# Optimization experiments

Hardware: AMD Instinct MI355X
Metric: run time of the kernel (lower is better)

## Reference

```python
import jax, jax.numpy as jnp
import numpy as np

N = 100000   # nodes
E = 1600000  # edges (before self loops)
IN, HID, OUT = 128, 128, 64


def setup_inputs() -> dict:
    key = jax.random.key(0)
    ks = jax.random.split(key, 5)
    x = jax.random.normal(ks[0], (N, IN), dtype=jnp.float32)
    edge_index = jax.random.randint(ks[1], (2, E), 0, N, dtype=jnp.int32)
    W1 = jax.random.normal(ks[2], (IN, HID), dtype=jnp.float32) * (1.0 / np.sqrt(IN))
    b1 = jnp.zeros((HID,), dtype=jnp.float32)
    W2 = jax.random.normal(ks[3], (HID, OUT), dtype=jnp.float32) * (1.0 / np.sqrt(HID))
    b2 = jnp.zeros((OUT,), dtype=jnp.float32)
    return {"x": x, "edge_index": edge_index, "W1": W1, "b1": b1, "W2": W2, "b2": b2}


def _gcn_conv(x, W, b, src, dst, norm):
    # linear transform first (small GEMM), then normalized scatter-add aggregation
    h = x @ W                                   # [N, d_out]
    msg = h[src] * norm[:, None]                # [E+N, d_out] gathered messages
    agg = jax.ops.segment_sum(msg, dst, num_segments=N)
    return agg + b


def reference(x, edge_index, W1, b1, W2, b2):
    loops = jnp.arange(N, dtype=edge_index.dtype)
    src = jnp.concatenate([edge_index[0], loops])   # add self loops (PyG GCNConv default)
    dst = jnp.concatenate([edge_index[1], loops])
    # symmetric normalization D^{-1/2} (A+I) D^{-1/2}
    deg = jax.ops.segment_sum(jnp.ones_like(dst, dtype=x.dtype), dst, num_segments=N)
    dinv = jnp.where(deg > 0, jax.lax.rsqrt(deg), 0.0)
    norm = dinv[src] * dinv[dst]                # [E+N]

    h = _gcn_conv(x, W1, b1, src, dst, norm)
    h = jax.nn.relu(h)
    out = _gcn_conv(h, W2, b2, src, dst, norm)
    return out
```

## Files before the change

### kernel.cpp

```cpp
#include <hip/hip_runtime.h>
#include <hip/hip_bf16.h>

#define IN_DIM  128
#define HID_DIM 128
#define OUT_DIM 64

typedef unsigned short ushort_t;
struct ushort4_t { ushort_t x, y, z, w; };
typedef __attribute__((ext_vector_type(8))) short bf16x8;
typedef __attribute__((ext_vector_type(4))) float f32x4;

__device__ __forceinline__ float bf2f(ushort_t u) {
    return __uint_as_float(((unsigned int)u) << 16);
}
__device__ __forceinline__ short f2bf_s(float v) {
    __hip_bfloat16 t = __float2bfloat16(v);
    return *(short*)&t;
}
__device__ __forceinline__ unsigned int pack2(float a, float b) {
    return ((unsigned int)(ushort_t)f2bf_s(b) << 16) | (ushort_t)f2bf_s(a);
}

__global__ void count_rank(const int* __restrict__ dst, int E,
                           int* __restrict__ cnt, int* __restrict__ rank) {
    int e = blockIdx.x * blockDim.x + threadIdx.x;
    if (e < E) rank[e] = atomicAdd(&cnt[dst[e]], 1);
}

__global__ void make_dinv(const int* __restrict__ cnt, float* __restrict__ dinv, int N) {
    int i = blockIdx.x * blockDim.x + threadIdx.x;
    if (i < N) dinv[i] = rsqrtf((float)(cnt[i] + 1));
}

__global__ void scan_partial(const int* __restrict__ cnt, int* __restrict__ bsum, int N) {
    __shared__ int wsum[4];
    const int t = threadIdx.x;
    const int base = blockIdx.x * 2048 + t * 8;
    int s = 0;
    #pragma unroll
    for (int i = 0; i < 8; ++i) s += (base + i < N) ? ((cnt[base + i] + 3) & ~3) : 0;
    #pragma unroll
    for (int off = 32; off > 0; off >>= 1) s += __shfl_down(s, off);
    const int lane = t & 63, w = t >> 6;
    if (lane == 0) wsum[w] = s;
    __syncthreads();
    if (t == 0) bsum[blockIdx.x] = wsum[0] + wsum[1] + wsum[2] + wsum[3];
}

__global__ void scan_partials(int* __restrict__ bsum, int S) {
    const int t = threadIdx.x;
    int running = 0;
    for (int base = 0; base < S; base += 64) {
        int i = base + t;
        int v = (i < S) ? bsum[i] : 0;
        int incl = v;
        #pragma unroll
        for (int off = 1; off < 64; off <<= 1) {
            int u = __shfl_up(incl, off);
            if (t >= off) incl += u;
        }
        if (i < S) bsum[i] = running + incl - v;
        running += __shfl(incl, 63);
    }
}

__global__ void scan_write(const int* __restrict__ cnt, const int* __restrict__ bsum,
                           int* __restrict__ row_start, int N) {
    __shared__ int wsum[4];
    const int t = threadIdx.x;
    const int base = blockIdx.x * 2048 + t * 8;
    int v[8];
    #pragma unroll
    for (int i = 0; i < 8; ++i) v[i] = (base + i < N) ? ((cnt[base + i] + 3) & ~3) : 0;
    int s = v[0] + v[1] + v[2] + v[3] + v[4] + v[5] + v[6] + v[7];
    const int lane = t & 63, w = t >> 6;
    int incl = s;
    #pragma unroll
    for (int off = 1; off < 64; off <<= 1) {
        int u = __shfl_up(incl, off);
        if (lane >= off) incl += u;
    }
    if (lane == 63) wsum[w] = incl;
    __syncthreads();
    int woff = 0;
    for (int i = 0; i < w; ++i) woff += wsum[i];
    int run = bsum[blockIdx.x] + woff + (incl - s);
    #pragma unroll
    for (int i = 0; i < 8; ++i) {
        if (base + i < N) row_start[base + i] = run;
        run += v[i];
    }
}

__global__ void fill_pack(const int* __restrict__ src, const int* __restrict__ dst,
                          const int* __restrict__ rank, const int* __restrict__ row_start,
                          const float* __restrict__ dinv, int E, int2* __restrict__ pack) {
    int e = blockIdx.x * blockDim.x + threadIdx.x;
    if (e < E) {
        int s = src[e], d = dst[e];
        int2 p;
        p.x = s;
        p.y = __float_as_int(dinv[s] * dinv[d]);
        pack[row_start[d] + rank[e]] = p;
    }
}

__global__ __launch_bounds__(256, 2) void gemm1_mfma(
        const float* __restrict__ x, const float* __restrict__ W,
        unsigned int* __restrict__ h, int N, int NT, int NW) {
    const int tid  = threadIdx.x;
    const int lane = tid & 63;
    const int m    = lane & 15;
    const int quad = lane >> 4;
    const int gw   = blockIdx.x * 4 + (tid >> 6);

    bf16x8 a[8][4];
    #pragma unroll
    for (int ct = 0; ct < 8; ++ct)
        #pragma unroll
        for (int kc = 0; kc < 4; ++kc)
            #pragma unroll
            for (int j = 0; j < 8; ++j)
                a[ct][kc][j] = f2bf_s(W[(size_t)(kc * 32 + quad * 8 + j) * HID_DIM + ct * 16 + m]);

    for (int t = gw; t < NT; t += NW) {
        const int n0 = t * 16;
        int node = n0 + m; if (node >= N) node = N - 1;
        const float* xr = x + (size_t)node * IN_DIM + quad * 8;
        f32x4 acc[8];
        #pragma unroll
        for (int ct = 0; ct < 8; ++ct) acc[ct] = (f32x4){0.f, 0.f, 0.f, 0.f};
        #pragma unroll
        for (int kc = 0; kc < 4; ++kc) {
            const float4 v0 = *(const float4*)(xr + kc * 32);
            const float4 v1 = *(const float4*)(xr + kc * 32 + 4);
            bf16x8 b;
            b[0] = f2bf_s(v0.x); b[1] = f2bf_s(v0.y); b[2] = f2bf_s(v0.z); b[3] = f2bf_s(v0.w);
            b[4] = f2bf_s(v1.x); b[5] = f2bf_s(v1.y); b[6] = f2bf_s(v1.z); b[7] = f2bf_s(v1.w);
            #pragma unroll
            for (int ct = 0; ct < 8; ++ct)
                acc[ct] = __builtin_amdgcn_mfma_f32_16x16x32_bf16(a[ct][kc], b, acc[ct], 0, 0, 0);
        }
        if (n0 + m < N) {
            unsigned int* o = h + (size_t)(n0 + m) * (HID_DIM / 2) + quad * 2;
            #pragma unroll
            for (int ct = 0; ct < 8; ++ct) {
                uint2 pv;
                pv.x = pack2(acc[ct][0], acc[ct][1]);
                pv.y = pack2(acc[ct][2], acc[ct][3]);
                *(uint2*)(o + ct * 8) = pv;
            }
        }
    }
}

__global__ __launch_bounds__(256) void gemm2_mfma(
        const ushort_t* __restrict__ agg, const float* __restrict__ b1,
        const float* __restrict__ W2, unsigned int* __restrict__ h2,
        int N, int NT, int NW) {
    const int tid  = threadIdx.x;
    const int lane = tid & 63;
    const int m    = lane & 15;
    const int quad = lane >> 4;
    const int gw   = blockIdx.x * 4 + (tid >> 6);

    bf16x8 a[4][4];
    #pragma unroll
    for (int ct = 0; ct < 4; ++ct)
        #pragma unroll
        for (int kc = 0; kc < 4; ++kc)
            #pragma unroll
            for (int j = 0; j < 8; ++j)
                a[ct][kc][j] = f2bf_s(W2[(size_t)(kc * 32 + quad * 8 + j) * OUT_DIM + ct * 16 + m]);

    float4 b1v[8];
    #pragma unroll
    for (int kc = 0; kc < 4; ++kc) {
        b1v[kc * 2]     = *(const float4*)(b1 + kc * 32 + quad * 8);
        b1v[kc * 2 + 1] = *(const float4*)(b1 + kc * 32 + quad * 8 + 4);
    }

    for (int t = gw; t < NT; t += NW) {
        const int n0 = t * 16;
        int node = n0 + m; if (node >= N) node = N - 1;
        const ushort_t* ar = agg + (size_t)node * HID_DIM + quad * 8;
        f32x4 acc[4];
        #pragma unroll
        for (int ct = 0; ct < 4; ++ct) acc[ct] = (f32x4){0.f, 0.f, 0.f, 0.f};
        #pragma unroll
        for (int kc = 0; kc < 4; ++kc) {
            const ushort4_t r0 = *(const ushort4_t*)(ar + kc * 32);
            const ushort4_t r1 = *(const ushort4_t*)(ar + kc * 32 + 4);
            const float4 ba = b1v[kc * 2], bb = b1v[kc * 2 + 1];
            bf16x8 b;
            b[0] = f2bf_s(fmaxf(bf2f(r0.x) + ba.x, 0.f));
            b[1] = f2bf_s(fmaxf(bf2f(r0.y) + ba.y, 0.f));
            b[2] = f2bf_s(fmaxf(bf2f(r0.z) + ba.z, 0.f));
            b[3] = f2bf_s(fmaxf(bf2f(r0.w) + ba.w, 0.f));
            b[4] = f2bf_s(fmaxf(bf2f(r1.x) + bb.x, 0.f));
            b[5] = f2bf_s(fmaxf(bf2f(r1.y) + bb.y, 0.f));
            b[6] = f2bf_s(fmaxf(bf2f(r1.z) + bb.z, 0.f));
            b[7] = f2bf_s(fmaxf(bf2f(r1.w) + bb.w, 0.f));
            #pragma unroll
            for (int ct = 0; ct < 4; ++ct)
                acc[ct] = __builtin_amdgcn_mfma_f32_16x16x32_bf16(a[ct][kc], b, acc[ct], 0, 0, 0);
        }
        if (n0 + m < N) {
            unsigned int* o = h2 + (size_t)(n0 + m) * (OUT_DIM / 2) + quad * 2;
            #pragma unroll
            for (int ct = 0; ct < 4; ++ct) {
                uint2 pv;
                pv.x = pack2(acc[ct][0], acc[ct][1]);
                pv.y = pack2(acc[ct][2], acc[ct][3]);
                *(uint2*)(o + ct * 8) = pv;
            }
        }
    }
}

template<int D, bool BF16_OUT>
__global__ void gather_bf16(const ushort_t* __restrict__ h, const int2* __restrict__ pack,
                            const int* __restrict__ row_start, const int* __restrict__ cnt,
                            const float* __restrict__ dinv, const float* __restrict__ bias,
                            int N, void* __restrict__ outv) {
    const int TPN = D / 4;
    const int NPB = 256 / TPN;
    const int t = threadIdx.x;
    const int node = blockIdx.x * NPB + t / TPN;
    if (node >= N) return;
    const int f = (t & (TPN - 1)) * 4;
    const float dd = dinv[node];

    const ushort4_t self = *(const ushort4_t*)(h + (size_t)node * D + f);
    const float sn = dd * dd;
    float4 acc;
    acc.x = bf2f(self.x) * sn; acc.y = bf2f(self.y) * sn;
    acc.z = bf2f(self.z) * sn; acc.w = bf2f(self.w) * sn;
    if (bias) {
        const float4 b = *(const float4*)(bias + f);
        acc.x += b.x; acc.y += b.y; acc.z += b.z; acc.w += b.w;
    }

    const int2* pk = pack + row_start[node];
    const int cpad = (cnt[node] + 3) & ~3;
    for (int e = 0; e < cpad; e += 4) {
        const int4 a = *(const int4*)(pk + e);
        const int4 b = *(const int4*)(pk + e + 2);
        {
            const ushort4_t v = *(const ushort4_t*)(h + (size_t)a.x * D + f);
            const float n = __int_as_float(a.y);
            acc.x += bf2f(v.x) * n; acc.y += bf2f(v.y) * n;
            acc.z += bf2f(v.z) * n; acc.w += bf2f(v.w) * n;
        }
        {
            const ushort4_t v = *(const ushort4_t*)(h + (size_t)a.z * D + f);
            const float n = __int_as_float(a.w);
            acc.x += bf2f(v.x) * n; acc.y += bf2f(v.y) * n;
            acc.z += bf2f(v.z) * n; acc.w += bf2f(v.w) * n;
        }
        {
            const ushort4_t v = *(const ushort4_t*)(h + (size_t)b.x * D + f);
            const float n = __int_as_float(b.y);
            acc.x += bf2f(v.x) * n; acc.y += bf2f(v.y) * n;
            acc.z += bf2f(v.z) * n; acc.w += bf2f(v.w) * n;
        }
        {
            const ushort4_t v = *(const ushort4_t*)(h + (size_t)b.z * D + f);
            const float n = __int_as_float(b.w);
            acc.x += bf2f(v.x) * n; acc.y += bf2f(v.y) * n;
            acc.z += bf2f(v.z) * n; acc.w += bf2f(v.w) * n;
        }
    }
    if (BF16_OUT) {
        unsigned int* out = (unsigned int*)outv;
        uint2 pv;
        pv.x = pack2(acc.x, acc.y);
        pv.y = pack2(acc.z, acc.w);
        *(uint2*)(out + ((size_t)node * D + f) / 2) = pv;
    } else {
        float* out = (float*)outv;
        *(float4*)(out + (size_t)node * D + f) = acc;
    }
}

extern "C" void kernel_launch(void* const* d_in, const int* in_sizes, int n_in,
                              void* d_out, int out_size, void* d_ws, size_t ws_size,
                              hipStream_t stream) {
    const float* x   = (const float*)d_in[0];
    const int*   ei  = (const int*)  d_in[1];
    const float* W1  = (const float*)d_in[2];
    const float* b1  = (const float*)d_in[3];
    const float* W2  = (const float*)d_in[4];
    const float* b2  = (const float*)d_in[5];
    float* out = (float*)d_out;

    const int N = in_sizes[0] / IN_DIM;
    const int E = in_sizes[1] / 2;
    const int* src = ei;
    const int* dst = ei + E;

    const int PACK_CAP = E + 4 * N;
    float* dinv      = (float*)d_ws;
    int*   cnt       = (int*)(dinv + N);
    int*   row_start = cnt + N;
    int*   bsum      = row_start + N;
    size_t off       = (size_t)(3 * N + 1024);
    off = (off + 3) & ~(size_t)3;
    int2*  pack      = (int2*)((int*)d_ws + off);
    unsigned int* h1 = (unsigned int*)(pack + PACK_CAP);
    unsigned int* agg1 = h1 + (size_t)N * (HID_DIM / 2);
    int*   rank      = (int*)agg1;
    unsigned int* h2 = h1;

    const int B = 256;
    const int S = (N + 2047) / 2048;
    const int NT = (N + 15) / 16;

    hipMemsetAsync(cnt, 0, (size_t)N * sizeof(int), stream);
    hipMemsetAsync(pack, 0, (size_t)PACK_CAP * sizeof(int2), stream);
    count_rank<<<(E + B - 1) / B, B, 0, stream>>>(dst, E, cnt, rank);
    make_dinv<<<(N + B - 1) / B, B, 0, stream>>>(cnt, dinv, N);
    scan_partial<<<S, 256, 0, stream>>>(cnt, bsum, N);
    scan_partials<<<1, 64, 0, stream>>>(bsum, S);
    scan_write<<<S, 256, 0, stream>>>(cnt, bsum, row_start, N);
    fill_pack<<<(E + B - 1) / B, B, 0, stream>>>(src, dst, rank, row_start, dinv, E, pack);

    gemm1_mfma<<<512, 256, 0, stream>>>(x, W1, h1, N, NT, 512 * 4);

    gather_bf16<HID_DIM, true><<<(N + 7) / 8, 256, 0, stream>>>(
        (const ushort_t*)h1, pack, row_start, cnt, dinv, nullptr, N, (void*)agg1);

    gemm2_mfma<<<768, 256, 0, stream>>>(
        (const ushort_t*)agg1, b1, W2, h2, N, NT, 768 * 4);

    gather_bf16<OUT_DIM, false><<<(N + 15) / 16, 256, 0, stream>>>(
        (const ushort_t*)h2, pack, row_start, cnt, dinv, b2, N, (void*)out);
}
```

Baseline: 338.5 us.

## Co-schedule first GEMM with degree counting in one kernel, fuse dinv into scan

The first feature GEMM and the atomic degree count/rank pass now run in a single launch: odd blocks do the MFMA GEMM and even blocks do vectorised atomic counting, so the compute-bound and atomic-bound work overlap. The dinv computation is folded into the partial scan kernel, and the edge pack fill reads src/dst/rank as int4. This removes separate launches and lets the GEMM hide atomic latency. In exchange, only half as many waves now work on the GEMM, and the two halves may be unevenly balanced.

```diff
diff --git a/kernel.cpp b/kernel.cpp
--- a/kernel.cpp
+++ b/kernel.cpp
@@ -21,24 +21,92 @@
     return ((unsigned int)(ushort_t)f2bf_s(b) << 16) | (ushort_t)f2bf_s(a);
 }
 
-__global__ void count_rank(const int* __restrict__ dst, int E,
-                           int* __restrict__ cnt, int* __restrict__ rank) {
-    int e = blockIdx.x * blockDim.x + threadIdx.x;
-    if (e < E) rank[e] = atomicAdd(&cnt[dst[e]], 1);
-}
-
-__global__ void make_dinv(const int* __restrict__ cnt, float* __restrict__ dinv, int N) {
-    int i = blockIdx.x * blockDim.x + threadIdx.x;
-    if (i < N) dinv[i] = rsqrtf((float)(cnt[i] + 1));
-}
-
-__global__ void scan_partial(const int* __restrict__ cnt, int* __restrict__ bsum, int N) {
+__global__ __launch_bounds__(256, 2) void fused_gemm1_count(
+        const float* __restrict__ x, const float* __restrict__ W,
+        unsigned int* __restrict__ h,
+        const int* __restrict__ dst, int* __restrict__ cnt, int* __restrict__ rank,
+        int N, int E, int NT) {
+    const int bid = blockIdx.x;
+    const int tid = threadIdx.x;
+
+    if (bid & 1) {
+        const int lane = tid & 63;
+        const int m    = lane & 15;
+        const int quad = lane >> 4;
+        const int gw   = (bid >> 1) * 4 + (tid >> 6);
+        const int NW   = 1024;
+
+        bf16x8 a[8][4];
+        #pragma unroll
+        for (int ct = 0; ct < 8; ++ct)
+            #pragma unroll
+            for (int kc = 0; kc < 4; ++kc)
+                #pragma unroll
+                for (int j = 0; j < 8; ++j)
+                    a[ct][kc][j] = f2bf_s(W[(size_t)(kc * 32 + quad * 8 + j) * HID_DIM + ct * 16 + m]);
+
+        for (int t = gw; t < NT; t += NW) {
+            const int n0 = t * 16;
+            int node = n0 + m; if (node >= N) node = N - 1;
+            const float* xr = x + (size_t)node * IN_DIM + quad * 8;
+            f32x4 acc[8];
+            #pragma unroll
+            for (int ct = 0; ct < 8; ++ct) acc[ct] = (f32x4){0.f, 0.f, 0.f, 0.f};
+            #pragma unroll
+            for (int kc = 0; kc < 4; ++kc) {
+                const float4 v0 = *(const float4*)(xr + kc * 32);
+                const float4 v1 = *(const float4*)(xr + kc * 32 + 4);
+                bf16x8 b;
+                b[0] = f2bf_s(v0.x); b[1] = f2bf_s(v0.y); b[2] = f2bf_s(v0.z); b[3] = f2bf_s(v0.w);
+                b[4] = f2bf_s(v1.x); b[5] = f2bf_s(v1.y); b[6] = f2bf_s(v1.z); b[7] = f2bf_s(v1.w);
+                #pragma unroll
+                for (int ct = 0; ct < 8; ++ct)
+                    acc[ct] = __builtin_amdgcn_mfma_f32_16x16x32_bf16(a[ct][kc], b, acc[ct], 0, 0, 0);
+            }
+            if (n0 + m < N) {
+                unsigned int* o = h + (size_t)(n0 + m) * (HID_DIM / 2) + quad * 2;
+                #pragma unroll
+                for (int ct = 0; ct < 8; ++ct) {
+                    uint2 pv;
+                    pv.x = pack2(acc[ct][0], acc[ct][1]);
+                    pv.y = pack2(acc[ct][2], acc[ct][3]);
+                    *(uint2*)(o + ct * 8) = pv;
+                }
+            }
+        }
+    } else {
+        const int ct = (bid >> 1) * 256 + tid;
+        const int CT = 256 * 256;
+        const int nq = E >> 2;
+        const int4* d4 = (const int4*)dst;
+        for (int q = ct; q < nq; q += CT) {
+            const int4 d = d4[q];
+            int4 r;
+            r.x = atomicAdd(&cnt[d.x], 1);
+            r.y = atomicAdd(&cnt[d.y], 1);
+            r.z = atomicAdd(&cnt[d.z], 1);
+            r.w = atomicAdd(&cnt[d.w], 1);
+            ((int4*)rank)[q] = r;
+        }
+        for (int e = (nq << 2) + ct; e < E; e += CT)
+            rank[e] = atomicAdd(&cnt[dst[e]], 1);
+    }
+}
+
+__global__ void scan_partial(const int* __restrict__ cnt, int* __restrict__ bsum,
+                             float* __restrict__ dinv, int N) {
     __shared__ int wsum[4];
     const int t = threadIdx.x;
     const int base = blockIdx.x * 2048 + t * 8;
     int s = 0;
     #pragma unroll
-    for (int i = 0; i < 8; ++i) s += (base + i < N) ? ((cnt[base + i] + 3) & ~3) : 0;
+    for (int i = 0; i < 8; ++i) {
+        if (base + i < N) {
+            const int c = cnt[base + i];
+            dinv[base + i] = rsqrtf((float)(c + 1));
+            s += (c + 3) & ~3;
+        }
+    }
     #pragma unroll
     for (int off = 32; off > 0; off >>= 1) s += __shfl_down(s, off);
     const int lane = t & 63, w = t >> 6;
@@ -92,64 +160,30 @@
     }
 }
 
-__global__ void fill_pack(const int* __restrict__ src, const int* __restrict__ dst,
-                          const int* __restrict__ rank, const int* __restrict__ row_start,
-                          const float* __restrict__ dinv, int E, int2* __restrict__ pack) {
-    int e = blockIdx.x * blockDim.x + threadIdx.x;
-    if (e < E) {
-        int s = src[e], d = dst[e];
+__global__ void fill_pack4(const int* __restrict__ src, const int* __restrict__ dst,
+                           const int* __restrict__ rank, const int* __restrict__ row_start,
+                           const float* __restrict__ dinv, int E, int2* __restrict__ pack) {
+    const int q = blockIdx.x * blockDim.x + threadIdx.x;
+    const int nq = E >> 2;
+    if (q < nq) {
+        const int4 s = ((const int4*)src)[q];
+        const int4 d = ((const int4*)dst)[q];
+        const int4 r = ((const int4*)rank)[q];
         int2 p;
-        p.x = s;
-        p.y = __float_as_int(dinv[s] * dinv[d]);
-        pack[row_start[d] + rank[e]] = p;
-    }
-}
-
-__global__ __launch_bounds__(256, 2) void gemm1_mfma(
-        const float* __restrict__ x, const float* __restrict__ W,
-        unsigned int* __restrict__ h, int N, int NT, int NW) {
-    const int tid  = threadIdx.x;
-    const int lane = tid & 63;
-    const int m    = lane & 15;
-    const int quad = lane >> 4;
-    const int gw   = blockIdx.x * 4 + (tid >> 6);
-
-    bf16x8 a[8][4];
-    #pragma unroll
-    for (int ct = 0; ct < 8; ++ct)
-        #pragma unroll
-        for (int kc = 0; kc < 4; ++kc)
-            #pragma unroll
-            for (int j = 0; j < 8; ++j)
-                a[ct][kc][j] = f2bf_s(W[(size_t)(kc * 32 + quad * 8 + j) * HID_DIM + ct * 16 + m]);
-
-    for (int t = gw; t < NT; t += NW) {
-        const int n0 = t * 16;
-        int node = n0 + m; if (node >= N) node = N - 1;
-        const float* xr = x + (size_t)node * IN_DIM + quad * 8;
-        f32x4 acc[8];
-        #pragma unroll
-        for (int ct = 0; ct < 8; ++ct) acc[ct] = (f32x4){0.f, 0.f, 0.f, 0.f};
-        #pragma unroll
-        for (int kc = 0; kc < 4; ++kc) {
-            const float4 v0 = *(const float4*)(xr + kc * 32);
-            const float4 v1 = *(const float4*)(xr + kc * 32 + 4);
-            bf16x8 b;
-            b[0] = f2bf_s(v0.x); b[1] = f2bf_s(v0.y); b[2] = f2bf_s(v0.z); b[3] = f2bf_s(v0.w);
-            b[4] = f2bf_s(v1.x); b[5] = f2bf_s(v1.y); b[6] = f2bf_s(v1.z); b[7] = f2bf_s(v1.w);
-            #pragma unroll
-            for (int ct = 0; ct < 8; ++ct)
-                acc[ct] = __builtin_amdgcn_mfma_f32_16x16x32_bf16(a[ct][kc], b, acc[ct], 0, 0, 0);
-        }
-        if (n0 + m < N) {
-            unsigned int* o = h + (size_t)(n0 + m) * (HID_DIM / 2) + quad * 2;
-            #pragma unroll
-            for (int ct = 0; ct < 8; ++ct) {
-                uint2 pv;
-                pv.x = pack2(acc[ct][0], acc[ct][1]);
-                pv.y = pack2(acc[ct][2], acc[ct][3]);
-                *(uint2*)(o + ct * 8) = pv;
-            }
+        p.x = s.x; p.y = __float_as_int(dinv[s.x] * dinv[d.x]);
+        pack[row_start[d.x] + r.x] = p;
+        p.x = s.y; p.y = __float_as_int(dinv[s.y] * dinv[d.y]);
+        pack[row_start[d.y] + r.y] = p;
+        p.x = s.z; p.y = __float_as_int(dinv[s.z] * dinv[d.z]);
+        pack[row_start[d.z] + r.z] = p;
+        p.x = s.w; p.y = __float_as_int(dinv[s.w] * dinv[d.w]);
+        pack[row_start[d.w] + r.w] = p;
+    }
+    if (q == 0) {
+        for (int e = nq << 2; e < E; ++e) {
+            int2 p;
+            p.x = src[e]; p.y = __float_as_int(dinv[src[e]] * dinv[dst[e]]);
+            pack[row_start[dst[e]] + rank[e]] = p;
         }
     }
 }
@@ -318,14 +352,13 @@
 
     hipMemsetAsync(cnt, 0, (size_t)N * sizeof(int), stream);
     hipMemsetAsync(pack, 0, (size_t)PACK_CAP * sizeof(int2), stream);
-    count_rank<<<(E + B - 1) / B, B, 0, stream>>>(dst, E, cnt, rank);
-    make_dinv<<<(N + B - 1) / B, B, 0, stream>>>(cnt, dinv, N);
-    scan_partial<<<S, 256, 0, stream>>>(cnt, bsum, N);
+    fused_gemm1_count<<<512, 256, 0, stream>>>(x, W1, h1, dst, cnt, rank, N, E, NT);
+
+    scan_partial<<<S, 256, 0, stream>>>(cnt, bsum, dinv, N);
     scan_partials<<<1, 64, 0, stream>>>(bsum, S);
     scan_write<<<S, 256, 0, stream>>>(cnt, bsum, row_start, N);
-    fill_pack<<<(E + B - 1) / B, B, 0, stream>>>(src, dst, rank, row_start, dinv, E, pack);
-
-    gemm1_mfma<<<512, 256, 0, stream>>>(x, W1, h1, N, NT, 512 * 4);
+
+    fill_pack4<<<((E >> 2) + B - 1) / B, B, 0, stream>>>(src, dst, rank, row_start, dinv, E, pack);
 
     gather_bf16<HID_DIM, true><<<(N + 7) / 8, 256, 0, stream>>>(
         (const ushort_t*)h1, pack, row_start, cnt, dinv, nullptr, N, (void*)agg1);
```

After: 316.4 us. 1.07x faster.
